# Optimization experiments

Hardware: AMD Instinct MI355X
Metric: run time of the kernel (lower is better)

## Reference

```python
import jax, jax.numpy as jnp
import numpy as np

B, N, C = 16, 4096, 768
H = 12
D = C // H  # 64
SCALE = D ** -0.5


def setup_inputs() -> dict:
    key = jax.random.key(0)
    k1, k2, k3, k4 = jax.random.split(key, 4)
    x = jax.random.normal(k1, (B, N, C), dtype=jnp.float32)
    # packed qkv projection (bias=False): torch Linear(dim, 3*dim)
    w_qkv = jax.random.normal(k2, (C, 3 * C), dtype=jnp.float32) * 0.02
    # output projection Linear(dim, dim) with bias
    w_proj = jax.random.normal(k3, (C, C), dtype=jnp.float32) * 0.02
    b_proj = jax.random.normal(k4, (C,), dtype=jnp.float32) * 0.02
    return {"x": x, "w_qkv": w_qkv, "w_proj": w_proj, "b_proj": b_proj}


def reference(x, w_qkv, w_proj, b_proj):
    b, n, c = x.shape
    # packed qkv: [B,N,3C] -> [3,B,H,N,D]
    qkv = (x @ w_qkv).reshape(b, n, 3, H, D).transpose(2, 0, 3, 1, 4)
    q, k, v = qkv[0], qkv[1], qkv[2]  # each [B,H,N,D]
    # kernelized (linear) attention: kv = (k^T v) * scale  -> [B,H,D,D]
    kv = jnp.einsum("bhnd,bhne->bhde", k, v) * SCALE
    # out = gelu(q) @ gelu(kv)  (exact/erf gelu, matching torch F.gelu default)
    gq = jax.nn.gelu(q, approximate=False)
    gkv = jax.nn.gelu(kv, approximate=False)
    out = jnp.einsum("bhtd,bhde->bhte", gq, gkv)  # [B,H,N,D]
    out = out.transpose(0, 2, 1, 3).reshape(b, n, c)  # b t (h d)
    return out @ w_proj + b_proj
```

## Files before the change

kernel.cpp:

```cpp
#include <hip/hip_runtime.h>
#include <hip/hip_bf16.h>


typedef __attribute__((ext_vector_type(8))) short short8_t;
typedef __attribute__((ext_vector_type(4))) float f32x4_t;

typedef __attribute__((address_space(1))) void as1_void;
typedef __attribute__((address_space(3))) void as3_void;

__device__ __forceinline__ void gload_lds16(const void* g, void* l) {
    __builtin_amdgcn_global_load_lds(
        (as1_void*)(unsigned long long)(g),
        (as3_void*)(unsigned long long)(l), 16, 0, 0);
}

__device__ __forceinline__ float gelu_f(float x) {
    float x2 = x * x;
    float t = x * fmaf(0.0356774081f, x2, 0.7978845608f);
    float e = __expf(2.0f * t);
    float th = 1.0f - 2.0f / (e + 1.0f);
    return 0.5f * x * (1.0f + th);
}

__device__ __forceinline__ unsigned short to_bf16(float f) {
    __hip_bfloat16 h = __float2bfloat16(f);
    return *reinterpret_cast<unsigned short*>(&h);
}

__device__ __forceinline__ f32x4_t mfma16(short8_t a, short8_t b, f32x4_t c) {
    return __builtin_amdgcn_mfma_f32_16x16x32_bf16(a, b, c, 0, 0, 0);
}

__global__ __launch_bounds__(256) void k_cvt_bf16(const float* __restrict__ in,
                                                  unsigned short* __restrict__ out,
                                                  long n) {
    long i = (long)blockIdx.x * blockDim.x + threadIdx.x;
    long stride = (long)gridDim.x * blockDim.x;
    for (long idx = i * 4; idx < n; idx += stride * 4) {
        float4 v = *(const float4*)(in + idx);
        ushort4 o;
        o.x = to_bf16(v.x); o.y = to_bf16(v.y); o.z = to_bf16(v.z); o.w = to_bf16(v.w);
        *(ushort4*)(out + idx) = o;
    }
}

__global__ __launch_bounds__(256) void k_wqkvT(const float* __restrict__ w,
                                               unsigned short* __restrict__ wT) {
    int gid = blockIdx.x * 256 + threadIdx.x;
    int c = gid / 96, rblk = gid % 96;
    int r0 = rblk * 8;
    short8_t o;
#pragma unroll
    for (int i = 0; i < 8; ++i)
        o[i] = (short)to_bf16(w[(size_t)(r0 + i) * 2304 + c]);
    *(short8_t*)(wT + (size_t)c * 768 + r0) = o;
}

__global__ __launch_bounds__(256) void k_wprojT(const float* __restrict__ w,
                                                unsigned short* __restrict__ wT) {
    int gid = blockIdx.x * 256 + threadIdx.x;
    int c = gid / 96, rblk = gid % 96;
    int r0 = rblk * 8;
    short8_t o;
#pragma unroll
    for (int i = 0; i < 8; ++i)
        o[i] = (short)to_bf16(w[(size_t)(r0 + i) * 768 + c]);
    *(short8_t*)(wT + (size_t)c * 768 + r0) = o;
}

template<bool GELU_EPI, bool BATCHED_B, bool BF16_OUT, bool BIAS>
__global__ __launch_bounds__(512, 2)
void k_gemm256(const unsigned short* __restrict__ A, int lda,
               const unsigned short* __restrict__ Bt, int ldb,
               void* __restrict__ Cout, int ldc,
               const float* __restrict__ bias,
               int tiles_n, int K) {
    __shared__ __attribute__((aligned(16))) unsigned short lds[2][2][2][128 * 64];

    const int nwg = gridDim.x;
    int bid = blockIdx.x;
    bid = (bid & 7) * (nwg >> 3) + (bid >> 3);

    const int tn = bid % tiles_n, tm = bid / tiles_n;
    const int row0 = tm * 256, col0 = tn * 256;

    const unsigned short* Bb = Bt;
    if (BATCHED_B) Bb += (size_t)(row0 >> 12) * 768 * 768;

    const int tid = threadIdx.x;
    const int lane = tid & 63;
    const int w = tid >> 6;
    const int wm = w >> 2;
    const int wn = w & 3;
    const int lr = lane & 15, lg = lane >> 4;

    const int c0 = tid, c1 = 512 + tid;
    const int sr0 = c0 >> 3, sk0 = (c0 & 7) ^ (sr0 & 7);
    const int sr1 = c1 >> 3, sk1 = (c1 & 7) ^ (sr1 & 7);

    auto stageA = [&](int buf, int half, int kt) {
        const unsigned short* base = A + (size_t)(row0 + half * 128) * lda + kt * 64;
        gload_lds16(base + (size_t)sr0 * lda + sk0 * 8, &lds[0][buf][half][c0 * 8]);
        gload_lds16(base + (size_t)sr1 * lda + sk1 * 8, &lds[0][buf][half][c1 * 8]);
    };
    auto stageB = [&](int buf, int half, int kt) {
        const unsigned short* base = Bb + (size_t)(col0 + half * 128) * ldb + kt * 64;
        gload_lds16(base + (size_t)sr0 * ldb + sk0 * 8, &lds[1][buf][half][c0 * 8]);
        gload_lds16(base + (size_t)sr1 * ldb + sk1 * 8, &lds[1][buf][half][c1 * 8]);
    };
    auto ldA = [&](int buf, int mi, int ks) -> short8_t {
        int row = mi * 16 + lr;
        int kc = (ks * 4 + lg) ^ (row & 7);
        return *(const short8_t*)&lds[0][buf][wm][row * 64 + kc * 8];
    };
    auto ldB = [&](int buf, int nj, int ks) -> short8_t {
        int row = wn * 64 + nj * 16 + lr;
        int half = row >> 7, rl = row & 127;
        int kc = (ks * 4 + lg) ^ (rl & 7);
        return *(const short8_t*)&lds[1][buf][half][rl * 64 + kc * 8];
    };

    f32x4_t acc[8][4] = {};
    short8_t bfrag[4][2];
    short8_t afrP[2][4];

#define FENCE asm volatile("" ::: "memory")
#define MFMACL(r0i, par)                                                        \
    __builtin_amdgcn_s_setprio(1);                                              \
    _Pragma("unroll") for (int nj = 0; nj < 4; ++nj) {                          \
        acc[r0i][nj]     = mfma16(afrP[par][0], bfrag[nj][0], acc[r0i][nj]);    \
        acc[r0i][nj]     = mfma16(afrP[par][1], bfrag[nj][1], acc[r0i][nj]);    \
        acc[r0i + 1][nj] = mfma16(afrP[par][2], bfrag[nj][0], acc[r0i + 1][nj]);\
        acc[r0i + 1][nj] = mfma16(afrP[par][3], bfrag[nj][1], acc[r0i + 1][nj]);\
    }                                                                           \
    __builtin_amdgcn_s_setprio(0);

#define GROUP(cb, nb, tnx)                                                      \
    {                                 \
      afrP[0][0] = ldA(cb, 0, 0); afrP[0][1] = ldA(cb, 0, 1);                   \
      afrP[0][2] = ldA(cb, 1, 0); afrP[0][3] = ldA(cb, 1, 1);                   \
      afrP[1][0] = ldA(cb, 2, 0); afrP[1][1] = ldA(cb, 2, 1);                   \
      afrP[1][2] = ldA(cb, 3, 0); afrP[1][3] = ldA(cb, 3, 1);                   \
      asm volatile("s_waitcnt lgkmcnt(4)" ::: "memory");                        \
      __builtin_amdgcn_sched_barrier(0);                                        \
      MFMACL(0, 0)                                                              \
      stageB(cb, 0, tnx);                                                       \
      FENCE; __builtin_amdgcn_s_barrier(); FENCE;                               \
                                              \
      afrP[0][0] = ldA(cb, 4, 0); afrP[0][1] = ldA(cb, 4, 1);                   \
      afrP[0][2] = ldA(cb, 5, 0); afrP[0][3] = ldA(cb, 5, 1);                   \
      asm volatile("s_waitcnt lgkmcnt(4)" ::: "memory");                        \
      __builtin_amdgcn_sched_barrier(0);                                        \
      MFMACL(2, 1)                                                              \
      stageB(cb, 1, tnx);                                                       \
      FENCE; __builtin_amdgcn_s_barrier(); FENCE;                               \
                                              \
      afrP[1][0] = ldA(cb, 6, 0); afrP[1][1] = ldA(cb, 6, 1);                   \
      afrP[1][2] = ldA(cb, 7, 0); afrP[1][3] = ldA(cb, 7, 1);                   \
      asm volatile("s_waitcnt lgkmcnt(4)" ::: "memory");                        \
      __builtin_amdgcn_sched_barrier(0);                                        \
      MFMACL(4, 0)                                                              \
      asm volatile("s_waitcnt vmcnt(8)" ::: "memory");                          \
      FENCE; __builtin_amdgcn_s_barrier(); FENCE;                               \
       \
      asm volatile("s_waitcnt lgkmcnt(0)" ::: "memory");                        \
      __builtin_amdgcn_sched_barrier(0);                                        \
      MFMACL(6, 1)                                                              \
      _Pragma("unroll") for (int nj = 0; nj < 4; ++nj)                          \
          _Pragma("unroll") for (int ks = 0; ks < 2; ++ks)                      \
              bfrag[nj][ks] = ldB(nb, nj, ks);                                  \
      stageA(cb, 0, tnx); stageA(cb, 1, tnx);                                   \
      asm volatile("s_waitcnt vmcnt(8)" ::: "memory");                          \
      FENCE; __builtin_amdgcn_s_barrier(); FENCE;                               \
    }

    const int nt = K >> 6;
    const int niter = nt >> 1;

    stageA(0, 0, 0); stageA(0, 1, 0); stageB(0, 0, 0); stageB(0, 1, 0);
    asm volatile("s_waitcnt vmcnt(0)" ::: "memory");
    __builtin_amdgcn_s_barrier();
    FENCE;
    stageB(1, 0, 1); stageB(1, 1, 1); stageA(1, 0, 1); stageA(1, 1, 1);
#pragma unroll
    for (int nj = 0; nj < 4; ++nj)
#pragma unroll
        for (int ks = 0; ks < 2; ++ks)
            bfrag[nj][ks] = ldB(0, nj, ks);
    asm volatile("s_waitcnt lgkmcnt(0)" ::: "memory");
    FENCE;

    for (int it = 0; it < niter; ++it) {
        const int tA = (2 * it + 2 < nt) ? 2 * it + 2 : 0;
        const int tB = (2 * it + 3 < nt) ? 2 * it + 3 : 0;
        GROUP(0, 1, tA);
        GROUP(1, 0, tB);
    }
    asm volatile("s_waitcnt vmcnt(0)" ::: "memory");
#undef GROUP
#undef MFMACL
#undef FENCE

    const int rbase = row0 + wm * 128 + (lg << 2);
    const int cbase = col0 + wn * 64 + lr;
#pragma unroll
    for (int mi = 0; mi < 8; ++mi)
#pragma unroll
        for (int nj = 0; nj < 4; ++nj)
#pragma unroll
            for (int r = 0; r < 4; ++r) {
                int row = rbase + mi * 16 + r;
                int col = cbase + nj * 16;
                float v = acc[mi][nj][r];
                if (GELU_EPI) v = gelu_f(v);
                if (BIAS) v += bias[col];
                if (BF16_OUT)
                    ((unsigned short*)Cout)[(size_t)row * ldc + col] = to_bf16(v);
                else
                    ((float*)Cout)[(size_t)row * ldc + col] = v;
            }
}

__global__ __launch_bounds__(256) void k_G(const unsigned short* __restrict__ xb,
                                           unsigned short* __restrict__ Gst) {
    static const signed char TI[21] = {0,0,0,0,0,0,1,1,1,1,1,2,2,2,2,3,3,3,4,4,5};
    static const signed char TJ[21] = {0,1,2,3,4,5,1,2,3,4,5,2,3,4,5,3,4,5,4,5,5};
    int bid = blockIdx.x;
    bid = (bid & 7) * 42 + (bid >> 3);
    const int b = bid / 21, t = bid % 21;
    const int d0 = TI[t] * 128, e0 = TJ[t] * 128;
    const bool diag = (d0 == e0);
    const unsigned short* xB = xb + (size_t)b * 4096 * 768;

    __shared__ __attribute__((aligned(16))) unsigned short lds[2][2][128 * 64];

    const int tid = threadIdx.x, lane = tid & 63, w = tid >> 6;
    const int colg = tid & 15;
    const int rq8 = (tid >> 4) & 7;
    const int blk = tid >> 7;
    const int wm = w >> 1, wn = w & 1;
    const int lr = lane & 15, lg = lane >> 4;
    const int base0 = (blk ? e0 : d0) + colg * 8;
    const int tb = diag ? 0 : 1;
    const bool active = (!diag) || (blk == 0);

    f32x4_t acc[4][4] = {};
    short8_t ra[8];

    auto loadx = [&](int it) {
        if (!active) return;
        const size_t rbase = (size_t)(it * 64 + rq8 * 8) * 768 + base0;
#pragma unroll
        for (int rr = 0; rr < 8; ++rr)
            ra[rr] = *(const short8_t*)(xB + rbase + (size_t)rr * 768);
    };
    auto writes = [&](int buf) {
        if (!active) return;
#pragma unroll
        for (int j = 0; j < 8; ++j) {
            const int c = colg * 8 + j;
            const int sw3 = ((c & 7) ^ (c >> 3)) & 7;
            short8_t v;
#pragma unroll
            for (int rr = 0; rr < 8; ++rr) v[rr] = ra[rr][j];
            *(short8_t*)(&lds[buf][blk][c * 64 + ((rq8 ^ sw3) << 3)]) = v;
        }
    };
    auto ldfrag = [&](int buf, int tile, int cbase, int o) -> short8_t {
        const int c = cbase + lr;
        const int sw3 = ((c & 7) ^ (c >> 3)) & 7;
        return *(const short8_t*)(&lds[buf][tile][c * 64 + ((o ^ sw3) << 3)]);
    };

    loadx(0);
    writes(0);
    __syncthreads();

    for (int it = 0; it < 64; ++it) {
        const int buf = it & 1;
        if (it < 63) loadx(it + 1);
#pragma unroll
        for (int ks = 0; ks < 2; ++ks) {
            short8_t af[4], bf[4];
#pragma unroll
            for (int mi = 0; mi < 4; ++mi)
                af[mi] = ldfrag(buf, 0, wm * 64 + mi * 16, ks * 4 + lg);
#pragma unroll
            for (int nj = 0; nj < 4; ++nj)
                bf[nj] = ldfrag(buf, tb, wn * 64 + nj * 16, ks * 4 + lg);
#pragma unroll
            for (int mi = 0; mi < 4; ++mi)
#pragma unroll
                for (int nj = 0; nj < 4; ++nj)
                    acc[mi][nj] = mfma16(af[mi], bf[nj], acc[mi][nj]);
        }
        if (it < 63) writes(buf ^ 1);
        __syncthreads();
    }

    const int dbase = d0 + wm * 64 + (lg << 2);
    const int ebase = e0 + wn * 64 + lr;
#pragma unroll
    for (int mi = 0; mi < 4; ++mi)
#pragma unroll
        for (int nj = 0; nj < 4; ++nj)
#pragma unroll
            for (int r = 0; r < 4; ++r)
                Gst[((size_t)b * 768 + dbase + mi * 16 + r) * 768 + ebase + nj * 16] =
                    to_bf16(acc[mi][nj][r]);

    if (!diag) {
        unsigned short* T = &lds[0][0][0];
#pragma unroll
        for (int mi = 0; mi < 4; ++mi)
#pragma unroll
            for (int nj = 0; nj < 4; ++nj) {
                const int el = wn * 64 + nj * 16 + lr;
                const int sig = ((el ^ (el >> 3)) & 7) << 1;
                const int s = wm * 16 + mi * 4 + lg;
                uint2 pk;
                pk.x = (unsigned int)to_bf16(acc[mi][nj][0]) |
                       ((unsigned int)to_bf16(acc[mi][nj][1]) << 16);
                pk.y = (unsigned int)to_bf16(acc[mi][nj][2]) |
                       ((unsigned int)to_bf16(acc[mi][nj][3]) << 16);
                *(uint2*)(&T[el * 128 + ((s ^ sig) << 2)]) = pk;
            }
        __syncthreads();
#pragma unroll
        for (int i = 0; i < 8; ++i) {
            const int el = i * 16 + (tid >> 4);
            const int p = tid & 15;
            const int sig = ((el ^ (el >> 3)) & 7) << 1;
            short8_t v = *(const short8_t*)(&T[el * 128 + (((2 * p) ^ sig) << 2)]);
            *(short8_t*)(Gst + ((size_t)b * 768 + e0 + el) * 768 + d0 + p * 8) = v;
        }
    }
}

__global__ __launch_bounds__(256) void k_kvh(const unsigned short* __restrict__ wqkv_bf,
                                             const unsigned short* __restrict__ Tst,
                                             unsigned short* __restrict__ gkvb) {
    const int bh = blockIdx.x;
    const int b = bh / 12, h = bh % 12;
    const unsigned short* kptr = wqkv_bf + 768 + h * 64;
    const unsigned short* vptr = Tst + (size_t)b * 768 * 768 + h * 64;

    __shared__ __attribute__((aligned(16))) unsigned short kT[64 * 64];
    __shared__ __attribute__((aligned(16))) unsigned short vT[64 * 64];

    const int tid = threadIdx.x, lane = tid & 63, w = tid >> 6;
    const int np = tid >> 3;
    const int g = tid & 7;

    f32x4_t acc[4] = {};

    for (int it = 0; it < 12; ++it) {
        const size_t r = (size_t)(it * 64 + 2 * np);
        short8_t k0 = *(const short8_t*)(kptr + r * 2304 + g * 8);
        short8_t k1 = *(const short8_t*)(kptr + (r + 1) * 2304 + g * 8);
        short8_t v0 = *(const short8_t*)(vptr + r * 768 + g * 8);
        short8_t v1 = *(const short8_t*)(vptr + (r + 1) * 768 + g * 8);
        __syncthreads();
#pragma unroll
        for (int j = 0; j < 8; ++j) {
            const int d = g * 8 + j;
            const int e = d * 64 + ((2 * np) ^ (((d ^ (d >> 3)) & 7) << 3));
            *(unsigned int*)(kT + e) =
                (unsigned int)(unsigned short)k0[j] | ((unsigned int)(unsigned short)k1[j] << 16);
            *(unsigned int*)(vT + e) =
                (unsigned int)(unsigned short)v0[j] | ((unsigned int)(unsigned short)v1[j] << 16);
        }
        __syncthreads();
        const int lr = lane & 15, lg = lane >> 4;
#pragma unroll
        for (int ks = 0; ks < 2; ++ks) {
            const int d = w * 16 + lr;
            short8_t a = *(const short8_t*)(kT + d * 64 +
                (((ks * 4 + lg) ^ ((d ^ (d >> 3)) & 7)) << 3));
#pragma unroll
            for (int nj = 0; nj < 4; ++nj) {
                const int e2 = nj * 16 + lr;
                short8_t bf = *(const short8_t*)(vT + e2 * 64 +
                    (((ks * 4 + lg) ^ ((e2 ^ (e2 >> 3)) & 7)) << 3));
                acc[nj] = __builtin_amdgcn_mfma_f32_16x16x32_bf16(a, bf, acc[nj], 0, 0, 0);
            }
        }
    }

    unsigned short* pout = gkvb + (size_t)bh * 4096;
    const int rb2 = w * 16 + ((lane >> 4) << 2);
    const int cb = lane & 15;
#pragma unroll
    for (int nj = 0; nj < 4; ++nj)
#pragma unroll
        for (int r = 0; r < 4; ++r)
            pout[(rb2 + r) * 64 + nj * 16 + cb] = to_bf16(gelu_f(acc[nj][r] * 0.125f));
}

__global__ __launch_bounds__(256) void k_M(const unsigned short* __restrict__ gkvb,
                                           const unsigned short* __restrict__ wpT,
                                           unsigned short* __restrict__ MT) {
    __shared__ __attribute__((aligned(16))) unsigned short As[64 * 64];
    __shared__ __attribute__((aligned(16))) unsigned short Bs[256 * 64];

    const int bid = blockIdx.x;
    const int bh = bid / 3, ct = bid % 3;
    const int b = bh / 12, h = bh % 12;
    const int c0 = ct * 256;
    const int tid = threadIdx.x, lane = tid & 63, w = tid >> 6;
    const int lr = lane & 15, lg = lane >> 4;

    short8_t ra[2], rb[8];
#pragma unroll
    for (int i = 0; i < 2; ++i) {
        int ch = i * 256 + tid, row = ch >> 3, kc = ch & 7;
        ra[i] = *(const short8_t*)(gkvb + (size_t)bh * 4096 + row * 64 + kc * 8);
    }
#pragma unroll
    for (int i = 0; i < 8; ++i) {
        int ch = i * 256 + tid, row = ch >> 3, kc = ch & 7;
        rb[i] = *(const short8_t*)(wpT + (size_t)(c0 + row) * 768 + h * 64 + kc * 8);
    }
#pragma unroll
    for (int i = 0; i < 2; ++i) {
        int ch = i * 256 + tid, row = ch >> 3, kc = ch & 7;
        *(short8_t*)(As + row * 64 + ((kc ^ (row & 7)) * 8)) = ra[i];
    }
#pragma unroll
    for (int i = 0; i < 8; ++i) {
        int ch = i * 256 + tid, row = ch >> 3, kc = ch & 7;
        *(short8_t*)(Bs + row * 64 + ((kc ^ (row & 7)) * 8)) = rb[i];
    }
    __syncthreads();

    f32x4_t acc[4][4] = {};
#pragma unroll
    for (int ks = 0; ks < 2; ++ks) {
        short8_t a[4], bfr[4];
#pragma unroll
        for (int mi = 0; mi < 4; ++mi) {
            int row = mi * 16 + lr;
            a[mi] = *(const short8_t*)(As + row * 64 + (((ks * 4 + lg) ^ (row & 7)) * 8));
        }
#pragma unroll
        for (int nj = 0; nj < 4; ++nj) {
            int row = w * 64 + nj * 16 + lr;
            bfr[nj] = *(const short8_t*)(Bs + row * 64 + (((ks * 4 + lg) ^ (row & 7)) * 8));
        }
#pragma unroll
        for (int mi = 0; mi < 4; ++mi)
#pragma unroll
            for (int nj = 0; nj < 4; ++nj)
                acc[mi][nj] = __builtin_amdgcn_mfma_f32_16x16x32_bf16(a[mi], bfr[nj], acc[mi][nj], 0, 0, 0);
    }
    __syncthreads();

#pragma unroll
    for (int mi = 0; mi < 4; ++mi)
#pragma unroll
        for (int nj = 0; nj < 4; ++nj) {
            unsigned int w0 = (unsigned int)to_bf16(acc[mi][nj][0]) |
                              ((unsigned int)to_bf16(acc[mi][nj][1]) << 16);
            unsigned int w1 = (unsigned int)to_bf16(acc[mi][nj][2]) |
                              ((unsigned int)to_bf16(acc[mi][nj][3]) << 16);
            uint2 pk; pk.x = w0; pk.y = w1;
            *(uint2*)(Bs + (w * 64 + nj * 16 + lr) * 64 + mi * 16 + lg * 4) = pk;
        }
    __syncthreads();
#pragma unroll
    for (int i = 0; i < 8; ++i) {
        int ch = i * 256 + tid, cl = ch >> 3, dk = ch & 7;
        short8_t v = *(const short8_t*)(Bs + cl * 64 + dk * 8);
        *(short8_t*)(MT + ((size_t)(b * 768) + c0 + cl) * 768 + h * 64 + dk * 8) = v;
    }
}

extern "C" void kernel_launch(void* const* d_in, const int* in_sizes, int n_in,
                              void* d_out, int out_size, void* d_ws, size_t ws_size,
                              hipStream_t stream) {
    const float* x      = (const float*)d_in[0];
    const float* w_qkv  = (const float*)d_in[1];
    const float* w_proj = (const float*)d_in[2];
    const float* b_proj = (const float*)d_in[3];
    float* out = (float*)d_out;
    char* ws = (char*)d_ws;

    unsigned short* q_gelu  = (unsigned short*)(ws);
    unsigned short* wqkvT   = (unsigned short*)(ws + 100663296);
    unsigned short* wqkv_bf = (unsigned short*)(ws + 104202240);
    unsigned short* G_bf    = (unsigned short*)(ws + 107741184);
    unsigned short* T_bf    = (unsigned short*)(ws + 126615552);
    unsigned short* MT      = (unsigned short*)(ws + 145489920);
    unsigned short* xb   = (unsigned short*)d_out;
    unsigned short* gkvb = (unsigned short*)((char*)d_out + 134217728);
    unsigned short* wpT  = (unsigned short*)((char*)d_out + 136314880);

    k_cvt_bf16<<<2048, 256, 0, stream>>>(x, xb, 50331648L);
    k_cvt_bf16<<<432, 256, 0, stream>>>(w_qkv, wqkv_bf, 1769472L);
    k_wqkvT<<<864, 256, 0, stream>>>(w_qkv, wqkvT);
    k_wprojT<<<288, 256, 0, stream>>>(w_proj, wpT);
    k_gemm256<true, false, true, false><<<768, 512, 0, stream>>>(
        xb, 768, wqkvT, 768, q_gelu, 768, nullptr, 3, 768);
    k_G<<<336, 256, 0, stream>>>(xb, G_bf);
    k_gemm256<false, false, true, false><<<144, 512, 0, stream>>>(
        G_bf, 768, wqkvT + (size_t)1536 * 768, 768, T_bf, 768, nullptr, 3, 768);
    k_kvh<<<192, 256, 0, stream>>>(wqkv_bf, T_bf, gkvb);
    k_M<<<576, 256, 0, stream>>>(gkvb, wpT, MT);
    k_gemm256<false, true, false, true><<<768, 512, 0, stream>>>(
        q_gelu, 768, MT, 768, out, 768, b_proj, 3, 768);
}
```

Before: 394.8 us.

## Merge weight prep kernels, fuse kv-gelu into M, use 128-tile GEMM for T

Combines the three weight conversion/transpose kernels into one launch, fuses the k^T v + gelu kernel with the M = gelu(kv) @ Wproj kernel so gelu(kv) stays in LDS instead of going through global memory, and replaces the 256-tile GEMM for the small T product (144 blocks) with a simpler 128-tile GEMM launched with 576 blocks to fill more CUs. The goals are fewer launches, less global traffic and better occupancy on the small GEMM. The fused kvM kernel now loops over three column tiles serially per block, so it has less parallelism (192 blocks) than the separate k_M launch had.

```diff
diff --git a/kernel.cpp b/kernel.cpp
--- a/kernel.cpp
+++ b/kernel.cpp
@@ -44,28 +44,38 @@
     }
 }
 
-__global__ __launch_bounds__(256) void k_wqkvT(const float* __restrict__ w,
-                                               unsigned short* __restrict__ wT) {
-    int gid = blockIdx.x * 256 + threadIdx.x;
-    int c = gid / 96, rblk = gid % 96;
-    int r0 = rblk * 8;
-    short8_t o;
-#pragma unroll
-    for (int i = 0; i < 8; ++i)
-        o[i] = (short)to_bf16(w[(size_t)(r0 + i) * 2304 + c]);
-    *(short8_t*)(wT + (size_t)c * 768 + r0) = o;
-}
-
-__global__ __launch_bounds__(256) void k_wprojT(const float* __restrict__ w,
-                                                unsigned short* __restrict__ wT) {
-    int gid = blockIdx.x * 256 + threadIdx.x;
-    int c = gid / 96, rblk = gid % 96;
-    int r0 = rblk * 8;
-    short8_t o;
-#pragma unroll
-    for (int i = 0; i < 8; ++i)
-        o[i] = (short)to_bf16(w[(size_t)(r0 + i) * 768 + c]);
-    *(short8_t*)(wT + (size_t)c * 768 + r0) = o;
+__global__ __launch_bounds__(256) void k_wprep(const float* __restrict__ w_qkv,
+                                               const float* __restrict__ w_proj,
+                                               unsigned short* __restrict__ wqkvT,
+                                               unsigned short* __restrict__ wpT,
+                                               unsigned short* __restrict__ wqkv_bf) {
+    const int blk = blockIdx.x, tid = threadIdx.x;
+    if (blk < 864) {
+        int gid = blk * 256 + tid;
+        int c = gid / 96, r0 = (gid % 96) * 8;
+        short8_t o;
+#pragma unroll
+        for (int i = 0; i < 8; ++i)
+            o[i] = (short)to_bf16(w_qkv[(size_t)(r0 + i) * 2304 + c]);
+        *(short8_t*)(wqkvT + (size_t)c * 768 + r0) = o;
+    } else if (blk < 1152) {
+        int gid = (blk - 864) * 256 + tid;
+        int c = gid / 96, r0 = (gid % 96) * 8;
+        short8_t o;
+#pragma unroll
+        for (int i = 0; i < 8; ++i)
+            o[i] = (short)to_bf16(w_proj[(size_t)(r0 + i) * 768 + c]);
+        *(short8_t*)(wpT + (size_t)c * 768 + r0) = o;
+    } else {
+        long i = (long)(blk - 1152) * 256 + tid;
+        long stride = 432L * 256;
+        for (long idx = i * 4; idx < 1769472L; idx += stride * 4) {
+            float4 v = *(const float4*)(w_qkv + idx);
+            ushort4 o;
+            o.x = to_bf16(v.x); o.y = to_bf16(v.y); o.z = to_bf16(v.z); o.w = to_bf16(v.w);
+            *(ushort4*)(wqkv_bf + idx) = o;
+        }
+    }
 }
 
 template<bool GELU_EPI, bool BATCHED_B, bool BF16_OUT, bool BIAS>
@@ -136,8 +146,7 @@
     __builtin_amdgcn_s_setprio(0);
 
 #define GROUP(cb, nb, tnx)                                                      \
-    {                                 \
-      afrP[0][0] = ldA(cb, 0, 0); afrP[0][1] = ldA(cb, 0, 1);                   \
+    { afrP[0][0] = ldA(cb, 0, 0); afrP[0][1] = ldA(cb, 0, 1);                   \
       afrP[0][2] = ldA(cb, 1, 0); afrP[0][3] = ldA(cb, 1, 1);                   \
       afrP[1][0] = ldA(cb, 2, 0); afrP[1][1] = ldA(cb, 2, 1);                   \
       afrP[1][2] = ldA(cb, 3, 0); afrP[1][3] = ldA(cb, 3, 1);                   \
@@ -146,7 +155,6 @@
       MFMACL(0, 0)                                                              \
       stageB(cb, 0, tnx);                                                       \
       FENCE; __builtin_amdgcn_s_barrier(); FENCE;                               \
-                                              \
       afrP[0][0] = ldA(cb, 4, 0); afrP[0][1] = ldA(cb, 4, 1);                   \
       afrP[0][2] = ldA(cb, 5, 0); afrP[0][3] = ldA(cb, 5, 1);                   \
       asm volatile("s_waitcnt lgkmcnt(4)" ::: "memory");                        \
@@ -154,7 +162,6 @@
       MFMACL(2, 1)                                                              \
       stageB(cb, 1, tnx);                                                       \
       FENCE; __builtin_amdgcn_s_barrier(); FENCE;                               \
-                                              \
       afrP[1][0] = ldA(cb, 6, 0); afrP[1][1] = ldA(cb, 6, 1);                   \
       afrP[1][2] = ldA(cb, 7, 0); afrP[1][3] = ldA(cb, 7, 1);                   \
       asm volatile("s_waitcnt lgkmcnt(4)" ::: "memory");                        \
@@ -162,7 +169,6 @@
       MFMACL(4, 0)                                                              \
       asm volatile("s_waitcnt vmcnt(8)" ::: "memory");                          \
       FENCE; __builtin_amdgcn_s_barrier(); FENCE;                               \
-       \
       asm volatile("s_waitcnt lgkmcnt(0)" ::: "memory");                        \
       __builtin_amdgcn_sched_barrier(0);                                        \
       MFMACL(6, 1)                                                              \
@@ -221,6 +227,70 @@
             }
 }
 
+__global__ __launch_bounds__(256)
+void k_gemm128(const unsigned short* __restrict__ A, int lda,
+               const unsigned short* __restrict__ Bt, int ldb,
+               unsigned short* __restrict__ C, int ldc,
+               int tiles_n, int K) {
+    __shared__ __attribute__((aligned(16))) unsigned short As[128 * 64];
+    __shared__ __attribute__((aligned(16))) unsigned short Bs[128 * 64];
+
+    const int nwg = gridDim.x;
+    int bid = blockIdx.x;
+    bid = (bid & 7) * (nwg >> 3) + (bid >> 3);
+
+    const int tn = bid % tiles_n, tm = bid / tiles_n;
+    const int row0 = tm * 128, col0 = tn * 128;
+
+    const int tid = threadIdx.x, lane = tid & 63, w = tid >> 6;
+    const int wm = w >> 1, wn = w & 1;
+    const int lr = lane & 15, lg = lane >> 4;
+
+    f32x4_t acc[4][4] = {};
+
+    const int nt = K >> 6;
+    for (int kt = 0; kt < nt; ++kt) {
+#pragma unroll
+        for (int i = 0; i < 4; ++i) {
+            int ch = i * 256 + tid;
+            int sr = ch >> 3, sk = (ch & 7) ^ (sr & 7);
+            gload_lds16(A + (size_t)(row0 + sr) * lda + kt * 64 + sk * 8, As + ch * 8);
+            gload_lds16(Bt + (size_t)(col0 + sr) * ldb + kt * 64 + sk * 8, Bs + ch * 8);
+        }
+        __syncthreads();
+#pragma unroll
+        for (int ks = 0; ks < 2; ++ks) {
+            short8_t a[4], b[4];
+#pragma unroll
+            for (int mi = 0; mi < 4; ++mi) {
+                int row = wm * 64 + mi * 16 + lr;
+                a[mi] = *(const short8_t*)(As + row * 64 + (((ks * 4 + lg) ^ (row & 7)) << 3));
+            }
+#pragma unroll
+            for (int nj = 0; nj < 4; ++nj) {
+                int row = wn * 64 + nj * 16 + lr;
+                b[nj] = *(const short8_t*)(Bs + row * 64 + (((ks * 4 + lg) ^ (row & 7)) << 3));
+            }
+#pragma unroll
+            for (int mi = 0; mi < 4; ++mi)
+#pragma unroll
+                for (int nj = 0; nj < 4; ++nj)
+                    acc[mi][nj] = mfma16(a[mi], b[nj], acc[mi][nj]);
+        }
+        __syncthreads();
+    }
+
+    const int rbase = row0 + wm * 64 + (lg << 2);
+    const int cbase = col0 + wn * 64 + lr;
+#pragma unroll
+    for (int mi = 0; mi < 4; ++mi)
+#pragma unroll
+        for (int nj = 0; nj < 4; ++nj)
+#pragma unroll
+            for (int r = 0; r < 4; ++r)
+                C[(size_t)(rbase + mi * 16 + r) * ldc + cbase + nj * 16] = to_bf16(acc[mi][nj][r]);
+}
+
 __global__ __launch_bounds__(256) void k_G(const unsigned short* __restrict__ xb,
                                            unsigned short* __restrict__ Gst) {
     static const signed char TI[21] = {0,0,0,0,0,0,1,1,1,1,1,2,2,2,2,3,3,3,4,4,5};
@@ -337,9 +407,10 @@
     }
 }
 
-__global__ __launch_bounds__(256) void k_kvh(const unsigned short* __restrict__ wqkv_bf,
+__global__ __launch_bounds__(256) void k_kvM(const unsigned short* __restrict__ wqkv_bf,
                                              const unsigned short* __restrict__ Tst,
-                                             unsigned short* __restrict__ gkvb) {
+                                             const unsigned short* __restrict__ wpT,
+                                             unsigned short* __restrict__ MT) {
     const int bh = blockIdx.x;
     const int b = bh / 12, h = bh % 12;
     const unsigned short* kptr = wqkv_bf + 768 + h * 64;
@@ -347,10 +418,13 @@
 
     __shared__ __attribute__((aligned(16))) unsigned short kT[64 * 64];
     __shared__ __attribute__((aligned(16))) unsigned short vT[64 * 64];
+    __shared__ __attribute__((aligned(16))) unsigned short As[64 * 64];
+    __shared__ __attribute__((aligned(16))) unsigned short Bs[256 * 64];
 
     const int tid = threadIdx.x, lane = tid & 63, w = tid >> 6;
     const int np = tid >> 3;
     const int g = tid & 7;
+    const int lr = lane & 15, lg = lane >> 4;
 
     f32x4_t acc[4] = {};
 
@@ -371,7 +445,6 @@
                 (unsigned int)(unsigned short)v0[j] | ((unsigned int)(unsigned short)v1[j] << 16);
         }
         __syncthreads();
-        const int lr = lane & 15, lg = lane >> 4;
 #pragma unroll
         for (int ks = 0; ks < 2; ++ks) {
             const int d = w * 16 + lr;
@@ -387,91 +460,75 @@
         }
     }
 
-    unsigned short* pout = gkvb + (size_t)bh * 4096;
-    const int rb2 = w * 16 + ((lane >> 4) << 2);
-    const int cb = lane & 15;
-#pragma unroll
-    for (int nj = 0; nj < 4; ++nj)
-#pragma unroll
-        for (int r = 0; r < 4; ++r)
-            pout[(rb2 + r) * 64 + nj * 16 + cb] = to_bf16(gelu_f(acc[nj][r] * 0.125f));
-}
-
-__global__ __launch_bounds__(256) void k_M(const unsigned short* __restrict__ gkvb,
-                                           const unsigned short* __restrict__ wpT,
-                                           unsigned short* __restrict__ MT) {
-    __shared__ __attribute__((aligned(16))) unsigned short As[64 * 64];
-    __shared__ __attribute__((aligned(16))) unsigned short Bs[256 * 64];
-
-    const int bid = blockIdx.x;
-    const int bh = bid / 3, ct = bid % 3;
-    const int b = bh / 12, h = bh % 12;
-    const int c0 = ct * 256;
-    const int tid = threadIdx.x, lane = tid & 63, w = tid >> 6;
-    const int lr = lane & 15, lg = lane >> 4;
-
-    short8_t ra[2], rb[8];
-#pragma unroll
-    for (int i = 0; i < 2; ++i) {
-        int ch = i * 256 + tid, row = ch >> 3, kc = ch & 7;
-        ra[i] = *(const short8_t*)(gkvb + (size_t)bh * 4096 + row * 64 + kc * 8);
-    }
-#pragma unroll
-    for (int i = 0; i < 8; ++i) {
-        int ch = i * 256 + tid, row = ch >> 3, kc = ch & 7;
-        rb[i] = *(const short8_t*)(wpT + (size_t)(c0 + row) * 768 + h * 64 + kc * 8);
-    }
-#pragma unroll
-    for (int i = 0; i < 2; ++i) {
-        int ch = i * 256 + tid, row = ch >> 3, kc = ch & 7;
-        *(short8_t*)(As + row * 64 + ((kc ^ (row & 7)) * 8)) = ra[i];
-    }
-#pragma unroll
-    for (int i = 0; i < 8; ++i) {
-        int ch = i * 256 + tid, row = ch >> 3, kc = ch & 7;
-        *(short8_t*)(Bs + row * 64 + ((kc ^ (row & 7)) * 8)) = rb[i];
-    }
-    __syncthreads();
-
-    f32x4_t acc[4][4] = {};
-#pragma unroll
-    for (int ks = 0; ks < 2; ++ks) {
-        short8_t a[4], bfr[4];
-#pragma unroll
-        for (int mi = 0; mi < 4; ++mi) {
-            int row = mi * 16 + lr;
-            a[mi] = *(const short8_t*)(As + row * 64 + (((ks * 4 + lg) ^ (row & 7)) * 8));
-        }
-#pragma unroll
-        for (int nj = 0; nj < 4; ++nj) {
-            int row = w * 64 + nj * 16 + lr;
-            bfr[nj] = *(const short8_t*)(Bs + row * 64 + (((ks * 4 + lg) ^ (row & 7)) * 8));
-        }
+    {
+        const int drow = w * 16 + (lg << 2);
+#pragma unroll
+        for (int nj = 0; nj < 4; ++nj)
+#pragma unroll
+            for (int r = 0; r < 4; ++r) {
+                const int d = drow + r;
+                const int e = nj * 16 + lr;
+                As[d * 64 + ((((e >> 3) ^ (d & 7)) << 3) | (e & 7))] =
+                    to_bf16(gelu_f(acc[nj][r] * 0.125f));
+            }
+    }
+
+    for (int ct = 0; ct < 3; ++ct) {
+        const int c0 = ct * 256;
+        short8_t rb[8];
+#pragma unroll
+        for (int i = 0; i < 8; ++i) {
+            int ch = i * 256 + tid, row = ch >> 3, kc = ch & 7;
+            rb[i] = *(const short8_t*)(wpT + (size_t)(c0 + row) * 768 + h * 64 + kc * 8);
+        }
+        __syncthreads();
+#pragma unroll
+        for (int i = 0; i < 8; ++i) {
+            int ch = i * 256 + tid, row = ch >> 3, kc = ch & 7;
+            *(short8_t*)(Bs + row * 64 + ((kc ^ (row & 7)) * 8)) = rb[i];
+        }
+        __syncthreads();
+
+        f32x4_t acc2[4][4] = {};
+#pragma unroll
+        for (int ks = 0; ks < 2; ++ks) {
+            short8_t a[4], bfr[4];
+#pragma unroll
+            for (int mi = 0; mi < 4; ++mi) {
+                int row = mi * 16 + lr;
+                a[mi] = *(const short8_t*)(As + row * 64 + (((ks * 4 + lg) ^ (row & 7)) * 8));
+            }
+#pragma unroll
+            for (int nj = 0; nj < 4; ++nj) {
+                int row = w * 64 + nj * 16 + lr;
+                bfr[nj] = *(const short8_t*)(Bs + row * 64 + (((ks * 4 + lg) ^ (row & 7)) * 8));
+            }
+#pragma unroll
+            for (int mi = 0; mi < 4; ++mi)
+#pragma unroll
+                for (int nj = 0; nj < 4; ++nj)
+                    acc2[mi][nj] = __builtin_amdgcn_mfma_f32_16x16x32_bf16(a[mi], bfr[nj], acc2[mi][nj], 0, 0, 0);
+        }
+        __syncthreads();
+
 #pragma unroll
         for (int mi = 0; mi < 4; ++mi)
 #pragma unroll
-            for (int nj = 0; nj < 4; ++nj)
-                acc[mi][nj] = __builtin_amdgcn_mfma_f32_16x16x32_bf16(a[mi], bfr[nj], acc[mi][nj], 0, 0, 0);
-    }
-    __syncthreads();
-
-#pragma unroll
-    for (int mi = 0; mi < 4; ++mi)
-#pragma unroll
-        for (int nj = 0; nj < 4; ++nj) {
-            unsigned int w0 = (unsigned int)to_bf16(acc[mi][nj][0]) |
-                              ((unsigned int)to_bf16(acc[mi][nj][1]) << 16);
-            unsigned int w1 = (unsigned int)to_bf16(acc[mi][nj][2]) |
-                              ((unsigned int)to_bf16(acc[mi][nj][3]) << 16);
-            uint2 pk; pk.x = w0; pk.y = w1;
-            *(uint2*)(Bs + (w * 64 + nj * 16 + lr) * 64 + mi * 16 + lg * 4) = pk;
-        }
-    __syncthreads();
-#pragma unroll
-    for (int i = 0; i < 8; ++i) {
-        int ch = i * 256 + tid, cl = ch >> 3, dk = ch & 7;
-        short8_t v = *(const short8_t*)(Bs + cl * 64 + dk * 8);
-        *(short8_t*)(MT + ((size_t)(b * 768) + c0 + cl) * 768 + h * 64 + dk * 8) = v;
+            for (int nj = 0; nj < 4; ++nj) {
+                unsigned int w0 = (unsigned int)to_bf16(acc2[mi][nj][0]) |
+                                  ((unsigned int)to_bf16(acc2[mi][nj][1]) << 16);
+                unsigned int w1 = (unsigned int)to_bf16(acc2[mi][nj][2]) |
+                                  ((unsigned int)to_bf16(acc2[mi][nj][3]) << 16);
+                uint2 pk; pk.x = w0; pk.y = w1;
+                *(uint2*)(Bs + (w * 64 + nj * 16 + lr) * 64 + mi * 16 + lg * 4) = pk;
+            }
+        __syncthreads();
+#pragma unroll
+        for (int i = 0; i < 8; ++i) {
+            int ch = i * 256 + tid, cl = ch >> 3, dk = ch & 7;
+            short8_t v = *(const short8_t*)(Bs + cl * 64 + dk * 8);
+            *(short8_t*)(MT + ((size_t)(b * 768) + c0 + cl) * 768 + h * 64 + dk * 8) = v;
+        }
     }
 }
 
@@ -492,20 +549,16 @@
     unsigned short* T_bf    = (unsigned short*)(ws + 126615552);
     unsigned short* MT      = (unsigned short*)(ws + 145489920);
     unsigned short* xb   = (unsigned short*)d_out;
-    unsigned short* gkvb = (unsigned short*)((char*)d_out + 134217728);
     unsigned short* wpT  = (unsigned short*)((char*)d_out + 136314880);
 
     k_cvt_bf16<<<2048, 256, 0, stream>>>(x, xb, 50331648L);
-    k_cvt_bf16<<<432, 256, 0, stream>>>(w_qkv, wqkv_bf, 1769472L);
-    k_wqkvT<<<864, 256, 0, stream>>>(w_qkv, wqkvT);
-    k_wprojT<<<288, 256, 0, stream>>>(w_proj, wpT);
+    k_wprep<<<1584, 256, 0, stream>>>(w_qkv, w_proj, wqkvT, wpT, wqkv_bf);
     k_gemm256<true, false, true, false><<<768, 512, 0, stream>>>(
         xb, 768, wqkvT, 768, q_gelu, 768, nullptr, 3, 768);
     k_G<<<336, 256, 0, stream>>>(xb, G_bf);
-    k_gemm256<false, false, true, false><<<144, 512, 0, stream>>>(
-        G_bf, 768, wqkvT + (size_t)1536 * 768, 768, T_bf, 768, nullptr, 3, 768);
-    k_kvh<<<192, 256, 0, stream>>>(wqkv_bf, T_bf, gkvb);
-    k_M<<<576, 256, 0, stream>>>(gkvb, wpT, MT);
+    k_gemm128<<<576, 256, 0, stream>>>(
+        G_bf, 768, wqkvT + (size_t)1536 * 768, 768, T_bf, 768, 6, 768);
+    k_kvM<<<192, 256, 0, stream>>>(wqkv_bf, T_bf, wpT, MT);
     k_gemm256<false, true, false, true><<<768, 512, 0, stream>>>(
         q_gelu, 768, MT, 768, out, 768, b_proj, 3, 768);
 }
```

New measurement: 386.1 us. 1.02x faster.
